# Kernel tuning notes

Hardware: AMD Instinct MI355X
Metric: run time of the kernel (lower is better)

The kernel has to match this reference:

```python
import jax, jax.numpy as jnp
import numpy as np
import math

N_HEADS = 16
D_Q = 1024
D_K = 1024
D_V = 1024
D_OUT = 1024
HID = D_OUT // N_HEADS  # 64
BATCH = 2
SEQ = 2048


def setup_inputs() -> dict:
    key = jax.random.key(0)
    ks = jax.random.split(key, 7)
    stdv = 1.0 / math.sqrt(HID)
    so = 1.0 / math.sqrt(D_OUT)
    return {
        "q": jax.random.normal(ks[0], (BATCH, SEQ, D_Q), dtype=jnp.float32),
        "k": jax.random.normal(ks[1], (BATCH, SEQ, D_K), dtype=jnp.float32),
        "v": jax.random.normal(ks[2], (BATCH, SEQ, D_V), dtype=jnp.float32),
        "W_query": jax.random.uniform(ks[3], (N_HEADS, D_Q, HID), jnp.float32, -stdv, stdv),
        "W_key": jax.random.uniform(ks[4], (N_HEADS, D_K, HID), jnp.float32, -stdv, stdv),
        "W_val": jax.random.uniform(ks[5], (N_HEADS, D_V, HID), jnp.float32, -stdv, stdv),
        "W_out": jax.random.uniform(ks[6], (N_HEADS, HID, D_OUT), jnp.float32, -so, so),
    }


def reference(q, k, v, W_query, W_key, W_val, W_out):
    norm = 1.0 / math.sqrt(HID)
    # per-head projections: [h, b, s, e]
    Q = jnp.einsum("bqd,hde->hbqe", q, W_query)
    K = jnp.einsum("bkd,hde->hbke", k, W_key)
    V = jnp.einsum("bkd,hde->hbke", v, W_val)
    # scaled dot-product attention
    compat = norm * jnp.einsum("hbqe,hbke->hbqk", Q, K)
    attn = jax.nn.softmax(compat, axis=-1)
    heads = jnp.einsum("hbqk,hbke->hbqe", attn, V)
    # output projection: concat heads then W_out == sum over h of per-head proj
    out = jnp.einsum("hbqe,heo->bqo", heads, W_out)
    return out
```

## Files before the change

### kernel.cpp

```cpp
#include <hip/hip_runtime.h>
#include <hip/hip_bf16.h>

typedef __bf16 bf16;
typedef __bf16 bf16x8 __attribute__((ext_vector_type(8)));
typedef __bf16 bf16x4 __attribute__((ext_vector_type(4)));
typedef float  f32x4  __attribute__((ext_vector_type(4)));

#define MFMA16(a,b,c) __builtin_amdgcn_mfma_f32_16x16x32_bf16(a, b, c, 0, 0, 0)

__device__ __forceinline__ void gl2lds16(const bf16* g, bf16* l) {
    __builtin_amdgcn_global_load_lds(
        (__attribute__((address_space(1))) void*)g,
        (__attribute__((address_space(3))) void*)l, 16, 0, 0);
}

__global__ __launch_bounds__(256)
void cvt_kernel(const float* __restrict__ s0, const float* __restrict__ s1,
                const float* __restrict__ s2, bf16* __restrict__ out)
{
    int gidx = blockIdx.x * 256 + threadIdx.x;
    int t    = gidx >> 19;
    int off  = (gidx & 0x7FFFF) * 8;
    const float* src = (t == 0) ? s0 : (t == 1) ? s1 : s2;
    const float4 f0 = *(const float4*)&src[off];
    const float4 f1 = *(const float4*)&src[off + 4];
    bf16x8 p = { (bf16)f0.x, (bf16)f0.y, (bf16)f0.z, (bf16)f0.w,
                 (bf16)f1.x, (bf16)f1.y, (bf16)f1.z, (bf16)f1.w };
    *(bf16x8*)&out[(size_t)gidx * 8] = p;
}

__global__ __launch_bounds__(256)
void wqkv_transpose(const float* __restrict__ Wq, const float* __restrict__ Wk,
                    const float* __restrict__ Wv, bf16* __restrict__ out)
{
    __shared__ bf16 Tl[64][72];
    const int t = blockIdx.z >> 4, h = blockIdx.z & 15;
    const float* inp = ((t == 0) ? Wq : (t == 1) ? Wk : Wv) + (size_t)h * 65536;
    bf16* outp = out + (size_t)t * 1024 * 1024 + (size_t)h * 65536;
    const int r0 = blockIdx.x * 64;
    const int tid = threadIdx.x;

    #pragma unroll
    for (int i = 0; i < 2; i++) {
        int s = tid + i * 256;
        int r = s >> 3, c8 = (s & 7) * 8;
        const float* ap = &inp[(size_t)(r0 + r) * 64 + c8];
        float4 f0 = *(const float4*)ap;
        float4 f1 = *(const float4*)(ap + 4);
        bf16x8 p = { (bf16)f0.x, (bf16)f0.y, (bf16)f0.z, (bf16)f0.w,
                     (bf16)f1.x, (bf16)f1.y, (bf16)f1.z, (bf16)f1.w };
        *(bf16x8*)&Tl[r][c8] = p;
    }
    __syncthreads();
    #pragma unroll
    for (int i = 0; i < 2; i++) {
        int s = tid + i * 256;
        int c = s >> 3, r8 = (s & 7) * 8;
        bf16x8 p;
        #pragma unroll
        for (int j = 0; j < 8; j++) p[j] = Tl[r8 + j][c];
        *(bf16x8*)&outp[(size_t)c * 1024 + r0 + r8] = p;
    }
}

__global__ __launch_bounds__(256)
void wo_transpose(const float* __restrict__ Wo, bf16* __restrict__ out)
{
    __shared__ bf16 Tl[64][72];
    const int h  = blockIdx.z;
    const int c0 = blockIdx.y * 64;
    const float* inp = Wo + (size_t)h * 65536;
    bf16* outp = out + (size_t)h * 64;
    const int tid = threadIdx.x;

    #pragma unroll
    for (int i = 0; i < 2; i++) {
        int s = tid + i * 256;
        int r = s >> 3, c8 = (s & 7) * 8;
        const float* ap = &inp[(size_t)r * 1024 + c0 + c8];
        float4 f0 = *(const float4*)ap;
        float4 f1 = *(const float4*)(ap + 4);
        bf16x8 p = { (bf16)f0.x, (bf16)f0.y, (bf16)f0.z, (bf16)f0.w,
                     (bf16)f1.x, (bf16)f1.y, (bf16)f1.z, (bf16)f1.w };
        *(bf16x8*)&Tl[r][c8] = p;
    }
    __syncthreads();
    #pragma unroll
    for (int i = 0; i < 2; i++) {
        int s = tid + i * 256;
        int c = s >> 3, r8 = (s & 7) * 8;
        bf16x8 p;
        #pragma unroll
        for (int j = 0; j < 8; j++) p[j] = Tl[r8 + j][c];
        *(bf16x8*)&outp[(size_t)(c0 + c) * 1024 + r8] = p;
    }
}

__global__ __launch_bounds__(256)
void qk_gemm(const bf16* __restrict__ Xcat, const bf16* __restrict__ Wqkv,
             bf16* __restrict__ Cq, bf16* __restrict__ Ck, float qscale)
{
    __shared__ bf16 Al[128 * 64];
    __shared__ bf16 Bl[128 * 64];
    const int slab  = blockIdx.x >> 5;
    const int mbase = (blockIdx.x & 31) * 128;
    const int nbase = blockIdx.y * 128;
    const int tid = threadIdx.x;
    const int w = tid >> 6, lane = tid & 63;
    const int lm = lane & 15, q4 = lane >> 4;
    const int wr = (w >> 1) * 64, wc = (w & 1) * 64;
    const int lrow = lane >> 3, lsw = ((lane & 7) ^ lrow) * 8;

    const bf16* A  = Xcat + (size_t)slab * 4096 * 1024;
    const bf16* Bt = Wqkv + (size_t)slab * 1024 * 1024;
    bf16* C = (slab == 0) ? Cq : Ck;
    const float scale = (slab == 0) ? qscale : 1.0f;

    f32x4 acc[4][4] = {};

    for (int k0 = 0; k0 < 1024; k0 += 64) {
        __syncthreads();
        #pragma unroll
        for (int i = 0; i < 4; i++) {
            int c = w * 4 + i;
            gl2lds16(&A [(size_t)(mbase + c * 8 + lrow) * 1024 + k0 + lsw], &Al[c * 512]);
            gl2lds16(&Bt[(size_t)(nbase + c * 8 + lrow) * 1024 + k0 + lsw], &Bl[c * 512]);
        }
        __syncthreads();
        #pragma unroll
        for (int kk2 = 0; kk2 < 2; kk2++) {
            bf16x8 a[4], bfr[4];
            const int g = ((kk2 * 4 + q4) ^ (lm & 7)) * 8;
            #pragma unroll
            for (int i = 0; i < 4; i++) a[i]   = *(const bf16x8*)&Al[(wr + i * 16 + lm) * 64 + g];
            #pragma unroll
            for (int j = 0; j < 4; j++) bfr[j] = *(const bf16x8*)&Bl[(wc + j * 16 + lm) * 64 + g];
            #pragma unroll
            for (int i = 0; i < 4; i++)
                #pragma unroll
                for (int j = 0; j < 4; j++)
                    acc[i][j] = MFMA16(a[i], bfr[j], acc[i][j]);
        }
    }

    #pragma unroll
    for (int i = 0; i < 4; i++)
        #pragma unroll
        for (int j = 0; j < 4; j++)
            #pragma unroll
            for (int r = 0; r < 4; r++) {
                int row = mbase + wr + i * 16 + q4 * 4 + r;
                int col = nbase + wc + j * 16 + lm;
                C[(size_t)row * 1024 + col] = (bf16)(acc[i][j][r] * scale);
            }
}

__global__ __launch_bounds__(256)
void v_gemm(const bf16* __restrict__ A, const bf16* __restrict__ Bt,
            bf16* __restrict__ Vt)
{
    __shared__ bf16 Al[128 * 64];
    __shared__ bf16 Bl[128 * 64];
    const int mbase = blockIdx.x * 128;
    const int nbase = blockIdx.y * 128;
    const int tid = threadIdx.x;
    const int w = tid >> 6, lane = tid & 63;
    const int lm = lane & 15, q4 = lane >> 4;
    const int wr = (w >> 1) * 64, wc = (w & 1) * 64;
    const int lrow = lane >> 3, lsw = ((lane & 7) ^ lrow) * 8;

    f32x4 acc[4][4] = {};

    for (int k0 = 0; k0 < 1024; k0 += 64) {
        __syncthreads();
        #pragma unroll
        for (int i = 0; i < 4; i++) {
            int c = w * 4 + i;
            gl2lds16(&A [(size_t)(mbase + c * 8 + lrow) * 1024 + k0 + lsw], &Al[c * 512]);
            gl2lds16(&Bt[(size_t)(nbase + c * 8 + lrow) * 1024 + k0 + lsw], &Bl[c * 512]);
        }
        __syncthreads();
        #pragma unroll
        for (int kk2 = 0; kk2 < 2; kk2++) {
            bf16x8 a[4], bfr[4];
            const int g = ((kk2 * 4 + q4) ^ (lm & 7)) * 8;
            #pragma unroll
            for (int i = 0; i < 4; i++) a[i]   = *(const bf16x8*)&Al[(wr + i * 16 + lm) * 64 + g];
            #pragma unroll
            for (int j = 0; j < 4; j++) bfr[j] = *(const bf16x8*)&Bl[(wc + j * 16 + lm) * 64 + g];
            #pragma unroll
            for (int i = 0; i < 4; i++)
                #pragma unroll
                for (int j = 0; j < 4; j++)
                    acc[i][j] = MFMA16(a[i], bfr[j], acc[i][j]);
        }
    }

    #pragma unroll
    for (int i = 0; i < 4; i++)
        #pragma unroll
        for (int j = 0; j < 4; j++) {
            int row = mbase + wr + i * 16 + q4 * 4;
            int col = nbase + wc + j * 16 + lm;
            bf16x4 p = { (bf16)acc[i][j][0], (bf16)acc[i][j][1],
                         (bf16)acc[i][j][2], (bf16)acc[i][j][3] };
            *(bf16x4*)&Vt[(size_t)col * 4096 + row] = p;
        }
}

__global__ __launch_bounds__(256)
void outproj_gemm(const bf16* __restrict__ A, const bf16* __restrict__ Bt,
                  float* __restrict__ C)
{
    __shared__ bf16 Al[128 * 64];
    __shared__ bf16 Bl[128 * 64];
    const int mbase = blockIdx.x * 128;
    const int nbase = blockIdx.y * 128;
    const int tid = threadIdx.x;
    const int w = tid >> 6, lane = tid & 63;
    const int lm = lane & 15, q4 = lane >> 4;
    const int wr = (w >> 1) * 64, wc = (w & 1) * 64;
    const int lrow = lane >> 3, lsw = ((lane & 7) ^ lrow) * 8;

    f32x4 acc[4][4] = {};

    for (int k0 = 0; k0 < 1024; k0 += 64) {
        __syncthreads();
        #pragma unroll
        for (int i = 0; i < 4; i++) {
            int c = w * 4 + i;
            gl2lds16(&A [(size_t)(mbase + c * 8 + lrow) * 1024 + k0 + lsw], &Al[c * 512]);
            gl2lds16(&Bt[(size_t)(nbase + c * 8 + lrow) * 1024 + k0 + lsw], &Bl[c * 512]);
        }
        __syncthreads();
        #pragma unroll
        for (int kk2 = 0; kk2 < 2; kk2++) {
            bf16x8 a[4], bfr[4];
            const int g = ((kk2 * 4 + q4) ^ (lm & 7)) * 8;
            #pragma unroll
            for (int i = 0; i < 4; i++) a[i]   = *(const bf16x8*)&Al[(wr + i * 16 + lm) * 64 + g];
            #pragma unroll
            for (int j = 0; j < 4; j++) bfr[j] = *(const bf16x8*)&Bl[(wc + j * 16 + lm) * 64 + g];
            #pragma unroll
            for (int i = 0; i < 4; i++)
                #pragma unroll
                for (int j = 0; j < 4; j++)
                    acc[i][j] = MFMA16(a[i], bfr[j], acc[i][j]);
        }
    }

    #pragma unroll
    for (int i = 0; i < 4; i++)
        #pragma unroll
        for (int j = 0; j < 4; j++)
            #pragma unroll
            for (int r = 0; r < 4; r++) {
                int row = mbase + wr + i * 16 + q4 * 4 + r;
                int col = nbase + wc + j * 16 + lm;
                C[(size_t)row * 1024 + col] = acc[i][j][r];
            }
}

__global__ __launch_bounds__(256)
void attn_kernel(const bf16* __restrict__ Qp, const bf16* __restrict__ Kp,
                 const bf16* __restrict__ Vt, bf16* __restrict__ Hd)
{
    __shared__ bf16 Kl[64 * 64];
    __shared__ bf16 Vl[64 * 64];
    __shared__ bf16 Pl[128][72];

    const int qt = blockIdx.x, b = blockIdx.y, h = blockIdx.z;
    const int qbase = qt * 128;
    const int tid  = threadIdx.x;
    const int w    = tid >> 6, lane = tid & 63;
    const int lm   = lane & 15, q4 = lane >> 4, kg = q4 * 8;
    const int lrow = lane >> 3, lsw = ((lane & 7) ^ lrow) * 8;

    bf16x8 Qf[2][2];
    #pragma unroll
    for (int i = 0; i < 2; i++)
        #pragma unroll
        for (int kk2 = 0; kk2 < 2; kk2++)
            Qf[i][kk2] = *(const bf16x8*)
                &Qp[(size_t)(b * 2048 + qbase + w * 32 + i * 16 + lm) * 1024
                    + h * 64 + kk2 * 32 + kg];

    f32x4 O[2][4] = {};
    float lsum[2][4] = {};

    const bf16* Kh = Kp + (size_t)(b * 2048) * 1024 + h * 64;
    const bf16* Vh = Vt + (size_t)(h * 64) * 4096 + b * 2048;

    for (int kt = 0; kt < 32; kt++) {
        __syncthreads();
        #pragma unroll
        for (int i = 0; i < 2; i++) {
            int c = w * 2 + i;
            gl2lds16(&Kh[(size_t)(kt * 64 + c * 8 + lrow) * 1024 + lsw], &Kl[c * 512]);
            gl2lds16(&Vh[(size_t)(c * 8 + lrow) * 4096 + kt * 64 + lsw], &Vl[c * 512]);
        }
        __syncthreads();

        f32x4 S[2][4] = {};
        #pragma unroll
        for (int kk2 = 0; kk2 < 2; kk2++) {
            bf16x8 bfr[4];
            const int g = ((kk2 * 4 + q4) ^ (lm & 7)) * 8;
            #pragma unroll
            for (int ct = 0; ct < 4; ct++)
                bfr[ct] = *(const bf16x8*)&Kl[(ct * 16 + lm) * 64 + g];
            #pragma unroll
            for (int i = 0; i < 2; i++)
                #pragma unroll
                for (int ct = 0; ct < 4; ct++)
                    S[i][ct] = MFMA16(Qf[i][kk2], bfr[ct], S[i][ct]);
        }

        #pragma unroll
        for (int i = 0; i < 2; i++)
            #pragma unroll
            for (int ct = 0; ct < 4; ct++)
                #pragma unroll
                for (int r = 0; r < 4; r++) {
                    float p = __builtin_amdgcn_exp2f(S[i][ct][r]);
                    lsum[i][r] += p;
                    Pl[w * 32 + i * 16 + q4 * 4 + r][ct * 16 + lm] = (bf16)p;
                }

        #pragma unroll
        for (int kk2 = 0; kk2 < 2; kk2++) {
            bf16x8 vfr[4];
            const int g = ((kk2 * 4 + q4) ^ (lm & 7)) * 8;
            #pragma unroll
            for (int et = 0; et < 4; et++)
                vfr[et] = *(const bf16x8*)&Vl[(et * 16 + lm) * 64 + g];
            #pragma unroll
            for (int i = 0; i < 2; i++) {
                bf16x8 a = *(const bf16x8*)&Pl[w * 32 + i * 16 + lm][kk2 * 32 + kg];
                #pragma unroll
                for (int et = 0; et < 4; et++)
                    O[i][et] = MFMA16(a, vfr[et], O[i][et]);
            }
        }
    }

    #pragma unroll
    for (int i = 0; i < 2; i++)
        #pragma unroll
        for (int r = 0; r < 4; r++) {
            float l = lsum[i][r];
            #pragma unroll
            for (int d = 1; d < 16; d <<= 1) l += __shfl_xor(l, d, 64);
            lsum[i][r] = 1.0f / l;
        }

    #pragma unroll
    for (int i = 0; i < 2; i++)
        #pragma unroll
        for (int et = 0; et < 4; et++)
            #pragma unroll
            for (int r = 0; r < 4; r++) {
                int row = b * 2048 + qbase + w * 32 + i * 16 + q4 * 4 + r;
                Hd[(size_t)row * 1024 + h * 64 + et * 16 + lm] = (bf16)(O[i][et][r] * lsum[i][r]);
            }
}

extern "C" void kernel_launch(void* const* d_in, const int* in_sizes, int n_in,
                              void* d_out, int out_size, void* d_ws, size_t ws_size,
                              hipStream_t stream)
{
    const float* q  = (const float*)d_in[0];
    const float* k  = (const float*)d_in[1];
    const float* v  = (const float*)d_in[2];
    const float* Wq = (const float*)d_in[3];
    const float* Wk = (const float*)d_in[4];
    const float* Wv = (const float*)d_in[5];
    const float* Wo = (const float*)d_in[6];
    float* out = (float*)d_out;

    const size_t Mi = 1024 * 1024;
    bf16* Xcat  = (bf16*)d_ws;
    bf16* Vtb   = Xcat;
    bf16* Hd    = Xcat + 4 * Mi;
    bf16* Wqkv  = Xcat + 12 * Mi;
    bf16* Wot   = Xcat + 15 * Mi;
    bf16* Qproj = Xcat + 16 * Mi;
    bf16* Kproj = Xcat + 20 * Mi;

    const float qscale = 0.125f * 1.4426950408889634f;

    cvt_kernel<<<6144, 256, 0, stream>>>(q, k, v, Xcat);

    wqkv_transpose<<<dim3(16, 1, 48), 256, 0, stream>>>(Wq, Wk, Wv, Wqkv);
    wo_transpose<<<dim3(1, 16, 16), 256, 0, stream>>>(Wo, Wot);

    qk_gemm<<<dim3(64, 8), 256, 0, stream>>>(Xcat, Wqkv, Qproj, Kproj, qscale);

    v_gemm<<<dim3(32, 8), 256, 0, stream>>>(Xcat + 8 * Mi, Wqkv + 2 * Mi, Vtb);

    attn_kernel<<<dim3(16, 2, 16), 256, 0, stream>>>(Qproj, Kproj, Vtb, Hd);

    outproj_gemm<<<dim3(32, 8), 256, 0, stream>>>(Hd, Wot, out);
}
```

Baseline: 235.6 us.

## Fuse Q/K/V projection GEMMs and restructure attention to keep P in registers

After: 254.8 us. 8.1% more time.

```diff
diff --git a/kernel.cpp b/kernel.cpp
--- a/kernel.cpp
+++ b/kernel.cpp
@@ -97,8 +97,9 @@
 }
 
 __global__ __launch_bounds__(256)
-void qk_gemm(const bf16* __restrict__ Xcat, const bf16* __restrict__ Wqkv,
-             bf16* __restrict__ Cq, bf16* __restrict__ Ck, float qscale)
+void qkv_gemm(const bf16* __restrict__ Xcat, const bf16* __restrict__ Wqkv,
+              bf16* __restrict__ Cq, bf16* __restrict__ Ck, bf16* __restrict__ Vt,
+              float qscale)
 {
     __shared__ bf16 Al[128 * 64];
     __shared__ bf16 Bl[128 * 64];
@@ -113,8 +114,6 @@
 
     const bf16* A  = Xcat + (size_t)slab * 4096 * 1024;
     const bf16* Bt = Wqkv + (size_t)slab * 1024 * 1024;
-    bf16* C = (slab == 0) ? Cq : Ck;
-    const float scale = (slab == 0) ? qscale : 1.0f;
 
     f32x4 acc[4][4] = {};
 
@@ -143,21 +142,36 @@
         }
     }
 
-    #pragma unroll
-    for (int i = 0; i < 4; i++)
-        #pragma unroll
-        for (int j = 0; j < 4; j++)
-            #pragma unroll
-            for (int r = 0; r < 4; r++) {
-                int row = mbase + wr + i * 16 + q4 * 4 + r;
+    if (slab == 2) {
+        #pragma unroll
+        for (int i = 0; i < 4; i++)
+            #pragma unroll
+            for (int j = 0; j < 4; j++) {
+                int row = mbase + wr + i * 16 + q4 * 4;
                 int col = nbase + wc + j * 16 + lm;
-                C[(size_t)row * 1024 + col] = (bf16)(acc[i][j][r] * scale);
-            }
-}
-
-__global__ __launch_bounds__(256)
-void v_gemm(const bf16* __restrict__ A, const bf16* __restrict__ Bt,
-            bf16* __restrict__ Vt)
+                bf16x4 p = { (bf16)acc[i][j][0], (bf16)acc[i][j][1],
+                             (bf16)acc[i][j][2], (bf16)acc[i][j][3] };
+                *(bf16x4*)&Vt[(size_t)col * 4096 + row] = p;
+            }
+    } else {
+        bf16* C = (slab == 0) ? Cq : Ck;
+        const float scale = (slab == 0) ? qscale : 1.0f;
+        #pragma unroll
+        for (int i = 0; i < 4; i++)
+            #pragma unroll
+            for (int j = 0; j < 4; j++)
+                #pragma unroll
+                for (int r = 0; r < 4; r++) {
+                    int row = mbase + wr + i * 16 + q4 * 4 + r;
+                    int col = nbase + wc + j * 16 + lm;
+                    C[(size_t)row * 1024 + col] = (bf16)(acc[i][j][r] * scale);
+                }
+    }
+}
+
+__global__ __launch_bounds__(256)
+void outproj_gemm(const bf16* __restrict__ A, const bf16* __restrict__ Bt,
+                  float* __restrict__ C)
 {
     __shared__ bf16 Al[128 * 64];
     __shared__ bf16 Bl[128 * 64];
@@ -199,59 +213,6 @@
     #pragma unroll
     for (int i = 0; i < 4; i++)
         #pragma unroll
-        for (int j = 0; j < 4; j++) {
-            int row = mbase + wr + i * 16 + q4 * 4;
-            int col = nbase + wc + j * 16 + lm;
-            bf16x4 p = { (bf16)acc[i][j][0], (bf16)acc[i][j][1],
-                         (bf16)acc[i][j][2], (bf16)acc[i][j][3] };
-            *(bf16x4*)&Vt[(size_t)col * 4096 + row] = p;
-        }
-}
-
-__global__ __launch_bounds__(256)
-void outproj_gemm(const bf16* __restrict__ A, const bf16* __restrict__ Bt,
-                  float* __restrict__ C)
-{
-    __shared__ bf16 Al[128 * 64];
-    __shared__ bf16 Bl[128 * 64];
-    const int mbase = blockIdx.x * 128;
-    const int nbase = blockIdx.y * 128;
-    const int tid = threadIdx.x;
-    const int w = tid >> 6, lane = tid & 63;
-    const int lm = lane & 15, q4 = lane >> 4;
-    const int wr = (w >> 1) * 64, wc = (w & 1) * 64;
-    const int lrow = lane >> 3, lsw = ((lane & 7) ^ lrow) * 8;
-
-    f32x4 acc[4][4] = {};
-
-    for (int k0 = 0; k0 < 1024; k0 += 64) {
-        __syncthreads();
-        #pragma unroll
-        for (int i = 0; i < 4; i++) {
-            int c = w * 4 + i;
-            gl2lds16(&A [(size_t)(mbase + c * 8 + lrow) * 1024 + k0 + lsw], &Al[c * 512]);
-            gl2lds16(&Bt[(size_t)(nbase + c * 8 + lrow) * 1024 + k0 + lsw], &Bl[c * 512]);
-        }
-        __syncthreads();
-        #pragma unroll
-        for (int kk2 = 0; kk2 < 2; kk2++) {
-            bf16x8 a[4], bfr[4];
-            const int g = ((kk2 * 4 + q4) ^ (lm & 7)) * 8;
-            #pragma unroll
-            for (int i = 0; i < 4; i++) a[i]   = *(const bf16x8*)&Al[(wr + i * 16 + lm) * 64 + g];
-            #pragma unroll
-            for (int j = 0; j < 4; j++) bfr[j] = *(const bf16x8*)&Bl[(wc + j * 16 + lm) * 64 + g];
-            #pragma unroll
-            for (int i = 0; i < 4; i++)
-                #pragma unroll
-                for (int j = 0; j < 4; j++)
-                    acc[i][j] = MFMA16(a[i], bfr[j], acc[i][j]);
-        }
-    }
-
-    #pragma unroll
-    for (int i = 0; i < 4; i++)
-        #pragma unroll
         for (int j = 0; j < 4; j++)
             #pragma unroll
             for (int r = 0; r < 4; r++) {
@@ -265,94 +226,96 @@
 void attn_kernel(const bf16* __restrict__ Qp, const bf16* __restrict__ Kp,
                  const bf16* __restrict__ Vt, bf16* __restrict__ Hd)
 {
-    __shared__ bf16 Kl[64 * 64];
-    __shared__ bf16 Vl[64 * 64];
-    __shared__ bf16 Pl[128][72];
+    __shared__ bf16 Vl[64 * 128];
 
     const int qt = blockIdx.x, b = blockIdx.y, h = blockIdx.z;
     const int qbase = qt * 128;
     const int tid  = threadIdx.x;
     const int w    = tid >> 6, lane = tid & 63;
-    const int lm   = lane & 15, q4 = lane >> 4, kg = q4 * 8;
-    const int lrow = lane >> 3, lsw = ((lane & 7) ^ lrow) * 8;
-
-    bf16x8 Qf[2][2];
-    #pragma unroll
-    for (int i = 0; i < 2; i++)
-        #pragma unroll
-        for (int kk2 = 0; kk2 < 2; kk2++)
-            Qf[i][kk2] = *(const bf16x8*)
-                &Qp[(size_t)(b * 2048 + qbase + w * 32 + i * 16 + lm) * 1024
-                    + h * 64 + kk2 * 32 + kg];
-
-    f32x4 O[2][4] = {};
-    float lsum[2][4] = {};
-
+    const int lm   = lane & 15, q4 = lane >> 4;
+
+    const bf16* Qh = Qp + (size_t)(b * 2048 + qbase + w * 32) * 1024 + h * 64;
     const bf16* Kh = Kp + (size_t)(b * 2048) * 1024 + h * 64;
     const bf16* Vh = Vt + (size_t)(h * 64) * 4096 + b * 2048;
 
-    for (int kt = 0; kt < 32; kt++) {
-        __syncthreads();
-        #pragma unroll
-        for (int i = 0; i < 2; i++) {
-            int c = w * 2 + i;
-            gl2lds16(&Kh[(size_t)(kt * 64 + c * 8 + lrow) * 1024 + lsw], &Kl[c * 512]);
-            gl2lds16(&Vh[(size_t)(c * 8 + lrow) * 4096 + kt * 64 + lsw], &Vl[c * 512]);
-        }
-        __syncthreads();
-
-        f32x4 S[2][4] = {};
-        #pragma unroll
-        for (int kk2 = 0; kk2 < 2; kk2++) {
-            bf16x8 bfr[4];
-            const int g = ((kk2 * 4 + q4) ^ (lm & 7)) * 8;
-            #pragma unroll
-            for (int ct = 0; ct < 4; ct++)
-                bfr[ct] = *(const bf16x8*)&Kl[(ct * 16 + lm) * 64 + g];
+    bf16x8 Qf[2][2];
+    #pragma unroll
+    for (int i = 0; i < 2; i++)
+        #pragma unroll
+        for (int kk2 = 0; kk2 < 2; kk2++)
+            Qf[i][kk2] = *(const bf16x8*)&Qh[(size_t)(i * 16 + lm) * 1024 + kk2 * 32 + q4 * 8];
+
+    f32x4 O[2][4] = {};
+    float lsum[2] = {};
+
+    const int vrow = lane >> 4;
+    const int vpg  = lane & 15;
+
+    for (int kt = 0; kt < 16; kt++) {
+        __syncthreads();
+        #pragma unroll
+        for (int i = 0; i < 4; i++) {
+            int c   = w * 4 + i;
+            int row = c * 4 + vrow;
+            int dg  = (vpg & 8) | ((vpg ^ row) & 7);
+            gl2lds16(&Vh[(size_t)row * 4096 + kt * 128 + dg * 8], &Vl[c * 512]);
+        }
+        __syncthreads();
+
+        #pragma unroll
+        for (int kk4 = 0; kk4 < 4; kk4++) {
+            f32x4 St[2][2] = {{{}, {}}, {{}, {}}};
+            #pragma unroll
+            for (int ctp = 0; ctp < 2; ctp++) {
+                int krow = kt * 128 + kk4 * 32 + ctp * 16 + lm;
+                #pragma unroll
+                for (int kk2 = 0; kk2 < 2; kk2++) {
+                    bf16x8 kf = *(const bf16x8*)
+                        &Kh[(size_t)krow * 1024 + kk2 * 32 + q4 * 8];
+                    #pragma unroll
+                    for (int i = 0; i < 2; i++)
+                        St[i][ctp] = MFMA16(kf, Qf[i][kk2], St[i][ctp]);
+                }
+            }
+            bf16x8 Pf[2];
             #pragma unroll
             for (int i = 0; i < 2; i++)
                 #pragma unroll
-                for (int ct = 0; ct < 4; ct++)
-                    S[i][ct] = MFMA16(Qf[i][kk2], bfr[ct], S[i][ct]);
-        }
-
-        #pragma unroll
-        for (int i = 0; i < 2; i++)
-            #pragma unroll
-            for (int ct = 0; ct < 4; ct++)
-                #pragma unroll
-                for (int r = 0; r < 4; r++) {
-                    float p = __builtin_amdgcn_exp2f(S[i][ct][r]);
-                    lsum[i][r] += p;
-                    Pl[w * 32 + i * 16 + q4 * 4 + r][ct * 16 + lm] = (bf16)p;
+                for (int j = 0; j < 8; j++) {
+                    float p = __builtin_amdgcn_exp2f(St[i][j >> 2][j & 3]);
+                    lsum[i] += p;
+                    Pf[i][j] = (bf16)p;
                 }
-
-        #pragma unroll
-        for (int kk2 = 0; kk2 < 2; kk2++) {
-            bf16x8 vfr[4];
-            const int g = ((kk2 * 4 + q4) ^ (lm & 7)) * 8;
-            #pragma unroll
-            for (int et = 0; et < 4; et++)
-                vfr[et] = *(const bf16x8*)&Vl[(et * 16 + lm) * 64 + g];
-            #pragma unroll
-            for (int i = 0; i < 2; i++) {
-                bf16x8 a = *(const bf16x8*)&Pl[w * 32 + i * 16 + lm][kk2 * 32 + kg];
-                #pragma unroll
-                for (int et = 0; et < 4; et++)
-                    O[i][et] = MFMA16(a, vfr[et], O[i][et]);
-            }
-        }
-    }
-
-    #pragma unroll
-    for (int i = 0; i < 2; i++)
+            #pragma unroll
+            for (int et = 0; et < 4; et++) {
+                int row = et * 16 + lm;
+                int dg1 = kk4 * 4 + (q4 >> 1);
+                int dg2 = dg1 + 2;
+                int pg1 = (dg1 & 8) | ((dg1 ^ row) & 7);
+                int pg2 = (dg2 & 8) | ((dg2 ^ row) & 7);
+                bf16x4 v0 = *(const bf16x4*)&Vl[row * 128 + pg1 * 8 + (q4 & 1) * 4];
+                bf16x4 v1 = *(const bf16x4*)&Vl[row * 128 + pg2 * 8 + (q4 & 1) * 4];
+                bf16x8 vf = { v0[0], v0[1], v0[2], v0[3],
+                              v1[0], v1[1], v1[2], v1[3] };
+                #pragma unroll
+                for (int i = 0; i < 2; i++)
+                    O[i][et] = MFMA16(Pf[i], vf, O[i][et]);
+            }
+        }
+    }
+
+    float rl[2][4];
+    #pragma unroll
+    for (int i = 0; i < 2; i++) {
+        float l = lsum[i];
+        l += __shfl_xor(l, 16, 64);
+        l += __shfl_xor(l, 32, 64);
         #pragma unroll
         for (int r = 0; r < 4; r++) {
-            float l = lsum[i][r];
-            #pragma unroll
-            for (int d = 1; d < 16; d <<= 1) l += __shfl_xor(l, d, 64);
-            lsum[i][r] = 1.0f / l;
-        }
+            float lr = __shfl(l, (lane & 48) + ((lane >> 4) & 3) * 4 + r, 64);
+            rl[i][r] = 1.0f / lr;
+        }
+    }
 
     #pragma unroll
     for (int i = 0; i < 2; i++)
@@ -361,7 +324,8 @@
             #pragma unroll
             for (int r = 0; r < 4; r++) {
                 int row = b * 2048 + qbase + w * 32 + i * 16 + q4 * 4 + r;
-                Hd[(size_t)row * 1024 + h * 64 + et * 16 + lm] = (bf16)(O[i][et][r] * lsum[i][r]);
+                Hd[(size_t)row * 1024 + h * 64 + et * 16 + lm] =
+                    (bf16)(O[i][et][r] * rl[i][r]);
             }
 }
 
@@ -380,23 +344,20 @@
 
     const size_t Mi = 1024 * 1024;
     bf16* Xcat  = (bf16*)d_ws;
-    bf16* Vtb   = Xcat;
-    bf16* Hd    = Xcat + 4 * Mi;
+    bf16* Hd    = Xcat;
     bf16* Wqkv  = Xcat + 12 * Mi;
     bf16* Wot   = Xcat + 15 * Mi;
     bf16* Qproj = Xcat + 16 * Mi;
     bf16* Kproj = Xcat + 20 * Mi;
+    bf16* Vtb   = (bf16*)d_out;
 
     const float qscale = 0.125f * 1.4426950408889634f;
 
     cvt_kernel<<<6144, 256, 0, stream>>>(q, k, v, Xcat);
-
     wqkv_transpose<<<dim3(16, 1, 48), 256, 0, stream>>>(Wq, Wk, Wv, Wqkv);
     wo_transpose<<<dim3(1, 16, 16), 256, 0, stream>>>(Wo, Wot);
 
-    qk_gemm<<<dim3(64, 8), 256, 0, stream>>>(Xcat, Wqkv, Qproj, Kproj, qscale);
-
-    v_gemm<<<dim3(32, 8), 256, 0, stream>>>(Xcat + 8 * Mi, Wqkv + 2 * Mi, Vtb);
+    qkv_gemm<<<dim3(96, 8), 256, 0, stream>>>(Xcat, Wqkv, Qproj, Kproj, Vtb, qscale);
 
     attn_kernel<<<dim3(16, 2, 16), 256, 0, stream>>>(Qproj, Kproj, Vtb, Hd);
 
```
